# Performance work log

Measured on AMD Instinct MI355X. Metric: run time of the kernel, lower is better.

The kernel has to match this reference:

```python
import jax, jax.numpy as jnp
import numpy as np

B, N, F, R = 8, 1024, 512, 32


def setup_inputs() -> dict:
    key = jax.random.key(0)
    kx, k1, k2, kg = jax.random.split(key, 4)
    scale = 0.02  # keep activations moderate (glorot-ish)
    return {
        "x": jax.random.normal(kx, (B, N, F), dtype=jnp.float32),
        "W1": jax.random.normal(k1, (F, R), dtype=jnp.float32) * scale,
        "W2": jax.random.normal(k2, (F, R), dtype=jnp.float32) * scale,
        "Wg": jax.random.normal(kg, (F, R), dtype=jnp.float32) * scale,
        "b": jnp.zeros((R,), dtype=jnp.float32),
    }


def reference(x, W1, W2, Wg, b):
    # Original math:
    #   z1[b,i,r] = (x @ W1 + bias)[b,i,r]
    #   z2[b,j,r] = (x @ W2)[b,j,r]
    #   g[b,j,r]  = (x @ Wg)[b,j,r]
    #   out[b,i,r] = sum_j (z1[b,i,r] + z2[b,j,r]) * g[b,j,r]
    # Algebraically identical fused form (avoids the [B,N,N,R] intermediate):
    #   out = z1 * sum_j g  +  sum_j (z2 * g)
    z1 = jnp.einsum("bnf,fr->bnr", x, W1) + b          # [B,N,R]
    z2 = jnp.einsum("bnf,fr->bnr", x, W2)              # [B,N,R]
    g = jnp.einsum("bnf,fr->bnr", x, Wg)               # [B,N,R]
    g_sum = jnp.sum(g, axis=1, keepdims=True)           # [B,1,R]
    z2g_sum = jnp.sum(z2 * g, axis=1, keepdims=True)    # [B,1,R]
    return z1 * g_sum + z2g_sum                          # [B,N,R]
```

## Files before the change

kernel.cpp:

```cpp
#include <hip/hip_runtime.h>
#include <hip/hip_bf16.h>

#define Bn 8
#define Nn 1024
#define Fn 512
#define Rn 32

typedef __attribute__((ext_vector_type(8))) short bf16x8;
typedef __attribute__((ext_vector_type(4))) float f32x4;

__global__ __launch_bounds__(256)
void kW(const float* __restrict__ W1, const float* __restrict__ W2,
        const float* __restrict__ Wg, short* __restrict__ Wt)
{
    __shared__ float xs[64 * 33];
    const int m  = blockIdx.x >> 3;
    const int f0 = (blockIdx.x & 7) * 64;
    const float* W = (m == 0) ? W1 : (m == 1) ? W2 : Wg;
    const int t = threadIdx.x;

    #pragma unroll
    for (int i = 0; i < 8; ++i) {
        int idx = t + i * 256;
        int fi = idx >> 5, r = idx & 31;
        xs[fi * 33 + r] = W[(size_t)(f0 + fi) * Rn + r];
    }
    __syncthreads();

    short* out = Wt + (size_t)m * (Rn * Fn);
    #pragma unroll
    for (int i = 0; i < 8; ++i) {
        int j = t + i * 256;
        int r = j >> 6, fi = j & 63;
        __hip_bfloat16 h = __float2bfloat16(xs[fi * 33 + r]);
        out[(size_t)r * Fn + f0 + fi] = *reinterpret_cast<short*>(&h);
    }
}

__global__ __launch_bounds__(64)
void k1(const float* __restrict__ x, const short* __restrict__ Wt,
        const float* __restrict__ bias, float* __restrict__ z1,
        float* __restrict__ gsum, float* __restrict__ z2gsum)
{
    const int l    = threadIdx.x;
    const int row0 = blockIdx.x * 16;
    const int bb   = row0 >> 10;
    const int lr   = l & 15;
    const int lk   = l >> 4;

    const float* xrow = x + (size_t)(row0 + lr) * Fn + 8 * lk;
    const short* w0   = Wt + 8 * lk;

    f32x4 acc1[2] = {}, acc2[2] = {}, accg[2] = {};

    #pragma unroll
    for (int kk = 0; kk < 16; ++kk) {
        float4 v0 = *(const float4*)(xrow + kk * 32);
        float4 v1 = *(const float4*)(xrow + kk * 32 + 4);
        float f[8] = {v0.x, v0.y, v0.z, v0.w, v1.x, v1.y, v1.z, v1.w};
        bf16x8 a;
        #pragma unroll
        for (int i = 0; i < 8; ++i) {
            __hip_bfloat16 h = __float2bfloat16(f[i]);
            a[i] = *reinterpret_cast<short*>(&h);
        }
        #pragma unroll
        for (int h = 0; h < 2; ++h) {
            const short* wp = w0 + (size_t)(h * 16 + lr) * Fn + kk * 32;
            bf16x8 b1 = *(const bf16x8*)(wp);
            bf16x8 b2 = *(const bf16x8*)(wp + 16384);
            bf16x8 bg = *(const bf16x8*)(wp + 32768);
            acc1[h] = __builtin_amdgcn_mfma_f32_16x16x32_bf16(a, b1, acc1[h], 0, 0, 0);
            acc2[h] = __builtin_amdgcn_mfma_f32_16x16x32_bf16(a, b2, acc2[h], 0, 0, 0);
            accg[h] = __builtin_amdgcn_mfma_f32_16x16x32_bf16(a, bg, accg[h], 0, 0, 0);
        }
    }

    const float bv[2] = {bias[lr], bias[16 + lr]};
    #pragma unroll
    for (int h = 0; h < 2; ++h) {
        #pragma unroll
        for (int reg = 0; reg < 4; ++reg) {
            int row = row0 + lk * 4 + reg;
            z1[(size_t)row * Rn + h * 16 + lr] = acc1[h][reg] + bv[h];
        }
    }

    float sg[2] = {0.f, 0.f}, sz[2] = {0.f, 0.f};
    #pragma unroll
    for (int h = 0; h < 2; ++h)
        #pragma unroll
        for (int reg = 0; reg < 4; ++reg) {
            float gv = accg[h][reg];
            sg[h] += gv;
            sz[h] += acc2[h][reg] * gv;
        }
    #pragma unroll
    for (int h = 0; h < 2; ++h) {
        sg[h] += __shfl_xor(sg[h], 16); sg[h] += __shfl_xor(sg[h], 32);
        sz[h] += __shfl_xor(sz[h], 16); sz[h] += __shfl_xor(sz[h], 32);
    }
    if (l < 16) {
        atomicAdd(&gsum[bb * Rn + lr],        sg[0]);
        atomicAdd(&gsum[bb * Rn + 16 + lr],   sg[1]);
        atomicAdd(&z2gsum[bb * Rn + lr],      sz[0]);
        atomicAdd(&z2gsum[bb * Rn + 16 + lr], sz[1]);
    }
}

__global__ __launch_bounds__(256)
void k2(const float4* __restrict__ z1, const float* __restrict__ gsum,
        const float* __restrict__ z2gsum, float4* __restrict__ out)
{
    const int i = blockIdx.x * 256 + threadIdx.x;
    const int e = i << 2;
    const int bb = e >> 15;
    const int rb = e & (Rn - 1);
    const float4 z  = z1[i];
    const float4 gs = *(const float4*)(gsum   + bb * Rn + rb);
    const float4 zg = *(const float4*)(z2gsum + bb * Rn + rb);
    float4 o;
    o.x = fmaf(z.x, gs.x, zg.x);
    o.y = fmaf(z.y, gs.y, zg.y);
    o.z = fmaf(z.z, gs.z, zg.z);
    o.w = fmaf(z.w, gs.w, zg.w);
    out[i] = o;
}

extern "C" void kernel_launch(void* const* d_in, const int* in_sizes, int n_in,
                              void* d_out, int out_size, void* d_ws, size_t ws_size,
                              hipStream_t stream)
{
    const float* x    = (const float*)d_in[0];
    const float* W1   = (const float*)d_in[1];
    const float* W2   = (const float*)d_in[2];
    const float* Wg   = (const float*)d_in[3];
    const float* bias = (const float*)d_in[4];
    float* out = (float*)d_out;

    short* Wt     = (short*)d_ws;
    float* z1     = (float*)((char*)d_ws + 3 * Rn * Fn * sizeof(short));
    float* gsum   = (float*)((char*)z1 + (size_t)Bn * Nn * Rn * sizeof(float));
    float* z2gsum = gsum + Bn * Rn;

    hipMemsetAsync(gsum, 0, 2 * Bn * Rn * sizeof(float), stream);

    kW<<<dim3(24), dim3(256), 0, stream>>>(W1, W2, Wg, Wt);

    k1<<<dim3((Bn * Nn) / 16), dim3(64), 0, stream>>>(
        x, Wt, bias, z1, gsum, z2gsum);

    k2<<<dim3((Bn * Nn * Rn / 4) / 256), dim3(256), 0, stream>>>(
        (const float4*)z1, gsum, z2gsum, (float4*)out);
}
```

Baseline: 83.38 us.

## Split K dimension of k1 across four waves with LDS reduction

Each block of k1 now uses four wavefronts, each computing a quarter of the F=512 reduction for the same 16 rows. Partial MFMA accumulators are combined through shared memory, then z1 is written and the per-block gsum/z2gsum partials are reduced before one atomic per column. The aim is to increase parallelism and memory-level concurrency per block and shorten each wave's serial K loop. The cost is extra LDS traffic, a 24KB shared buffer and barriers.

```diff
diff --git a/kernel.cpp b/kernel.cpp
--- a/kernel.cpp
+++ b/kernel.cpp
@@ -37,24 +37,27 @@
     }
 }
 
-__global__ __launch_bounds__(64)
+__global__ __launch_bounds__(256)
 void k1(const float* __restrict__ x, const short* __restrict__ Wt,
         const float* __restrict__ bias, float* __restrict__ z1,
         float* __restrict__ gsum, float* __restrict__ z2gsum)
 {
-    const int l    = threadIdx.x;
+    __shared__ float red[3][4][16][32];
+    const int t    = threadIdx.x;
+    const int l    = t & 63;
+    const int w    = t >> 6;
     const int row0 = blockIdx.x * 16;
     const int bb   = row0 >> 10;
     const int lr   = l & 15;
     const int lk   = l >> 4;
 
-    const float* xrow = x + (size_t)(row0 + lr) * Fn + 8 * lk;
-    const short* w0   = Wt + 8 * lk;
+    const float* xrow = x + (size_t)(row0 + lr) * Fn + w * 128 + 8 * lk;
+    const short* w0   = Wt + w * 128 + 8 * lk;
 
     f32x4 acc1[2] = {}, acc2[2] = {}, accg[2] = {};
 
     #pragma unroll
-    for (int kk = 0; kk < 16; ++kk) {
+    for (int kk = 0; kk < 4; ++kk) {
         float4 v0 = *(const float4*)(xrow + kk * 32);
         float4 v1 = *(const float4*)(xrow + kk * 32 + 4);
         float f[8] = {v0.x, v0.y, v0.z, v0.w, v1.x, v1.y, v1.z, v1.w};
@@ -76,35 +79,45 @@
         }
     }
 
-    const float bv[2] = {bias[lr], bias[16 + lr]};
-    #pragma unroll
-    for (int h = 0; h < 2; ++h) {
-        #pragma unroll
-        for (int reg = 0; reg < 4; ++reg) {
-            int row = row0 + lk * 4 + reg;
-            z1[(size_t)row * Rn + h * 16 + lr] = acc1[h][reg] + bv[h];
-        }
-    }
-
-    float sg[2] = {0.f, 0.f}, sz[2] = {0.f, 0.f};
     #pragma unroll
     for (int h = 0; h < 2; ++h)
         #pragma unroll
         for (int reg = 0; reg < 4; ++reg) {
-            float gv = accg[h][reg];
-            sg[h] += gv;
-            sz[h] += acc2[h][reg] * gv;
+            const int rr = lk * 4 + reg, cc = h * 16 + lr;
+            red[0][w][rr][cc] = acc1[h][reg];
+            red[1][w][rr][cc] = acc2[h][reg];
+            red[2][w][rr][cc] = accg[h][reg];
         }
+    __syncthreads();
+
+    const int col = t & 31, r0 = t >> 5;
+    float z1a = 0.f, z2a = 0.f, ga = 0.f, z1b = 0.f, z2b = 0.f, gb = 0.f;
     #pragma unroll
-    for (int h = 0; h < 2; ++h) {
-        sg[h] += __shfl_xor(sg[h], 16); sg[h] += __shfl_xor(sg[h], 32);
-        sz[h] += __shfl_xor(sz[h], 16); sz[h] += __shfl_xor(sz[h], 32);
+    for (int ww = 0; ww < 4; ++ww) {
+        z1a += red[0][ww][r0][col];     z1b += red[0][ww][r0 + 8][col];
+        z2a += red[1][ww][r0][col];     z2b += red[1][ww][r0 + 8][col];
+        ga  += red[2][ww][r0][col];     gb  += red[2][ww][r0 + 8][col];
     }
-    if (l < 16) {
-        atomicAdd(&gsum[bb * Rn + lr],        sg[0]);
-        atomicAdd(&gsum[bb * Rn + 16 + lr],   sg[1]);
-        atomicAdd(&z2gsum[bb * Rn + lr],      sz[0]);
-        atomicAdd(&z2gsum[bb * Rn + 16 + lr], sz[1]);
+    const float bv = bias[col];
+    z1[(size_t)(row0 + r0) * Rn + col]     = z1a + bv;
+    z1[(size_t)(row0 + r0 + 8) * Rn + col] = z1b + bv;
+
+    const float pg = ga + gb;
+    const float pz = z2a * ga + z2b * gb;
+    __syncthreads();
+    float* r2 = (float*)red;
+    r2[r0 * 32 + col]       = pg;
+    r2[256 + r0 * 32 + col] = pz;
+    __syncthreads();
+    if (t < 32) {
+        float sg = 0.f, sz = 0.f;
+        #pragma unroll
+        for (int i = 0; i < 8; ++i) {
+            sg += r2[i * 32 + t];
+            sz += r2[256 + i * 32 + t];
+        }
+        atomicAdd(&gsum[bb * Rn + t],   sg);
+        atomicAdd(&z2gsum[bb * Rn + t], sz);
     }
 }
 
@@ -147,7 +160,7 @@
 
     kW<<<dim3(24), dim3(256), 0, stream>>>(W1, W2, Wg, Wt);
 
-    k1<<<dim3((Bn * Nn) / 16), dim3(64), 0, stream>>>(
+    k1<<<dim3((Bn * Nn) / 16), dim3(256), 0, stream>>>(
         x, Wt, bias, z1, gsum, z2gsum);
 
     k2<<<dim3((Bn * Nn * Rn / 4) / 256), dim3(256), 0, stream>>>(
```

New measurement: 82.08 us. No clear change (-1.6%).
